# Performance work log

Hardware: AMD Instinct MI355X
Metric: run time of the kernel (lower is better)

Reference implementation:

```python
import jax, jax.numpy as jnp
import numpy as np

L, D, H, HD = 2, 2048, 16, 128          # layers, hidden, heads, head_dim
E, K, F, FS = 8, 2, 1408, 5632           # experts, top_k, moe_inter, shared_inter
V, T = 32000, 2048                       # vocab, tokens
EPS = 1e-6
ROPE_BASE = 1000000.0


def _rms(x, w):
    return x * jax.lax.rsqrt(jnp.mean(x * x, axis=-1, keepdims=True) + EPS) * w


def _rope(x, cos, sin):
    half = x.shape[-1] // 2
    x1, x2 = x[..., :half], x[..., half:]
    return jnp.concatenate([x1 * cos - x2 * sin, x1 * sin + x2 * cos], axis=-1)


def setup_inputs() -> dict:
    key = jax.random.key(0)
    ks = jax.random.split(key, 18)
    s = 0.02
    f = lambda k, shp: jax.random.normal(k, shp, jnp.float32) * s
    return {
        "input_ids": jax.random.randint(ks[0], (T,), 0, V, dtype=jnp.int32),
        "positions": jnp.arange(T, dtype=jnp.int32),
        "embed": f(ks[1], (V, D)),
        "qw": f(ks[2], (L, D, H * HD)),
        "kw": f(ks[3], (L, D, H * HD)),
        "vw": f(ks[4], (L, D, H * HD)),
        "ow": f(ks[5], (L, H * HD, D)),
        "ln1": jnp.ones((L, D), jnp.float32),
        "ln2": jnp.ones((L, D), jnp.float32),
        "router_w": f(ks[6], (L, D, E)),
        "sgate_w": f(ks[7], (L, D)),
        "wg": f(ks[8], (L, E, D, F)),
        "wu": f(ks[9], (L, E, D, F)),
        "wd": f(ks[10], (L, E, F, D)),
        "swg": f(ks[11], (L, D, FS)),
        "swu": f(ks[12], (L, D, FS)),
        "swd": f(ks[13], (L, FS, D)),
        "final_ln": jnp.ones((D,), jnp.float32),
    }


def _attn(x, positions, qw_l, kw_l, vw_l, ow_l):
    q = (x @ qw_l).reshape(T, H, HD)
    k = (x @ kw_l).reshape(T, H, HD)
    v = (x @ vw_l).reshape(T, H, HD)
    half = HD // 2
    inv = 1.0 / (ROPE_BASE ** (jnp.arange(half, dtype=jnp.float32) / half))
    ang = positions.astype(jnp.float32)[:, None] * inv[None, :]  # [T, half]
    cos, sin = jnp.cos(ang)[:, None, :], jnp.sin(ang)[:, None, :]
    q = _rope(q, cos, sin)
    k = _rope(k, cos, sin)
    scores = jnp.einsum('thd,shd->hts', q, k) * (HD ** -0.5)  # [H, T, T]
    mask = positions[:, None] >= positions[None, :]  # causal
    scores = jnp.where(mask[None], scores, -1e30)
    p = jax.nn.softmax(scores, axis=-1)
    o = jnp.einsum('hts,shd->thd', p, v).reshape(T, H * HD)
    return o @ ow_l


def _moe(x, router_w_l, sgate_w_l, wg_l, wu_l, wd_l, swg_l, swu_l, swd_l):
    # shared expert + its sigmoid gate
    sh = (jax.nn.silu(x @ swg_l) * (x @ swu_l)) @ swd_l
    sgate = jax.nn.sigmoid(x @ sgate_w_l)[:, None]
    # router: softmax in float32, then top-k with prob renorm (norm_topk_prob)
    probs = jax.nn.softmax((x @ router_w_l).astype(jnp.float32), axis=-1)
    topv, topi = jax.lax.top_k(probs, K)
    topv = topv / jnp.sum(topv, axis=-1, keepdims=True)
    combine = jnp.sum(jax.nn.one_hot(topi, E, dtype=x.dtype) * topv[..., None].astype(x.dtype), axis=1)  # [T, E]
    # dense grouped expert FFN, combined by routing weights (scatter-add equivalent)
    g = jnp.einsum('td,edf->etf', x, wg_l)
    u = jnp.einsum('td,edf->etf', x, wu_l)
    y = jnp.einsum('etf,efd->etd', jax.nn.silu(g) * u, wd_l)
    moe_out = jnp.einsum('te,etd->td', combine, y)
    return (moe_out + sgate * sh) * (1.0 / K ** 0.5)


def reference(input_ids, positions, embed, qw, kw, vw, ow, ln1, ln2, router_w,
              sgate_w, wg, wu, wd, swg, swu, swd, final_ln):
    h = embed[input_ids]  # [T, D]
    residual = None
    for l in range(L):
        if residual is None:
            residual = h
            x = _rms(h, ln1[l])
        else:
            residual = h + residual
            x = _rms(residual, ln1[l])
        h = _attn(x, positions, qw[l], kw[l], vw[l], ow[l])
        residual = h + residual
        x = _rms(residual, ln2[l])
        h = _moe(x, router_w[l], sgate_w[l], wg[l], wu[l], wd[l], swg[l], swu[l], swd[l])
    residual = h + residual
    return _rms(residual, final_ln)
```

## Files before the change

kernel.cpp:

```cpp
#include <hip/hip_runtime.h>
#include <stdint.h>

#define TT 2048
#define DD 2048
#define HH 16
#define HDIM 128
#define NE 8
#define TOPK 2
#define FF 1408
#define FSS 5632
#define NL 2

typedef __bf16 bf16;
typedef __bf16 bf16x2 __attribute__((ext_vector_type(2)));
typedef __bf16 bf16x4 __attribute__((ext_vector_type(4)));
typedef __bf16 bf16x8 __attribute__((ext_vector_type(8)));
typedef float f32x4 __attribute__((ext_vector_type(4)));

__device__ __forceinline__ void split1(float f, bf16& h, bf16& l) {
  bf16 hb = (bf16)f;
  h = hb;
  l = (bf16)(f - (float)hb);
}

__device__ __forceinline__ void gload16(const void* g, void* l) {
  __builtin_amdgcn_global_load_lds((const __attribute__((address_space(1))) void*)g,
                                   (__attribute__((address_space(3))) void*)l, 16, 0, 0);
}

template<bool LO>
__launch_bounds__(256)
__global__ void k_wtrans(const float* __restrict__ W, bf16* __restrict__ Wh,
                         bf16* __restrict__ Wl, int Kd, int N)
{
  __shared__ float T[64][68];
  const size_t slab = (size_t)blockIdx.z * (size_t)Kd * (size_t)N;
  const float* Wp = W + slab;
  const int k0 = blockIdx.x * 64, n0 = blockIdx.y * 64;
  const int tid = threadIdx.x;
  const int rr = tid >> 2, c4 = (tid & 3) * 4;
  const float* src = Wp + (size_t)(k0 + rr) * N + n0 + c4;
#pragma unroll
  for (int j = 0; j < 4; ++j) {
    f32x4 v = *(const f32x4*)(src + j * 16);
    *(f32x4*)&T[rr][c4 + j * 16] = v;
  }
  __syncthreads();
  const int nn = tid >> 2, kk = (tid & 3) * 16;
  bf16x8 h0, h1, l0, l1;
#pragma unroll
  for (int j = 0; j < 8; ++j) {
    bf16 hb, lb;
    split1(T[kk + j][nn], hb, lb);
    h0[j] = hb; l0[j] = lb;
    split1(T[kk + 8 + j][nn], hb, lb);
    h1[j] = hb; l1[j] = lb;
  }
  size_t out = slab + (size_t)(n0 + nn) * Kd + k0 + kk;
  *(bf16x8*)&Wh[out] = h0;
  *(bf16x8*)&Wh[out + 8] = h1;
  if (LO) {
    *(bf16x8*)&Wl[out] = l0;
    *(bf16x8*)&Wl[out + 8] = l1;
  }
}

template<int BMT, int NT, bool EXPERT, bool GATHER, int OM>
__launch_bounds__(256, (BMT == 128 ? 3 : 4))
__global__ void k_gemmp(const bf16* __restrict__ Ah, const bf16* __restrict__ Al,
                        const bf16* __restrict__ Bh, const bf16* __restrict__ Bl,
                        void* __restrict__ C1, void* __restrict__ C2,
                        int M, int N, int Kd, int lda, int ldc,
                        const int* __restrict__ perm, const int* __restrict__ cnt,
                        const int* __restrict__ ofs)
{
  constexpr int PL = (NT == 3) ? 2 : 1;
  constexpr int ASUB = BMT / 16;
  constexpr int AISS = PL * ASUB;
  constexpr int BISS = PL * 8;
  constexpr int QPW = (AISS + BISS) / 4;
  constexpr int IF = BMT / 32;

  int m_count = M, row_base = 0;
  size_t boff = 0;
  if (EXPERT) {
    int e = blockIdx.z;
    m_count = cnt[e];
    if ((int)(blockIdx.x * BMT) >= m_count) return;
    row_base = ofs[e];
    boff = (size_t)e * (size_t)N * (size_t)Kd;
  }
  const int tid = threadIdx.x, lane = tid & 63, wid = tid >> 6;
  const int wm = (wid >> 1) * (BMT / 2), wn = (wid & 1) * 64;
  const int lr = lane & 15, g = lane >> 4;
  const int n0 = blockIdx.y * 128;
  const int m0 = blockIdx.x * BMT;

  __shared__ bf16 As[PL][BMT][32];
  __shared__ bf16 Bs[PL][128][32];

  const bf16* srcp[QPW];
#pragma unroll
  for (int j = 0; j < QPW; ++j) {
    int q = wid * QPW + j;
    int r16 = lane >> 2;
    int kc = (lane & 3) ^ ((lane >> 3) & 3);
    if (q < AISS) {
      int pl = q / ASUB, sub = q % ASUB;
      int r = sub * 16 + r16;
      int tok;
      if (EXPERT) {
        int lrow = m0 + r;
        if (lrow >= m_count) lrow = m_count - 1;
        tok = GATHER ? perm[row_base + lrow] : (row_base + lrow);
      } else {
        tok = m0 + r;
      }
      const bf16* base = (pl == 0) ? Ah : Al;
      srcp[j] = base + (size_t)tok * lda + kc * 8;
    } else {
      int qb = q - AISS;
      int pl = qb >> 3, sub = qb & 7;
      int nrow = sub * 16 + r16;
      const bf16* base = (pl == 0) ? Bh : Bl;
      srcp[j] = base + boff + (size_t)(n0 + nrow) * Kd + kc * 8;
    }
  }

  f32x4 acc[IF][4];
#pragma unroll
  for (int i = 0; i < IF; ++i)
#pragma unroll
    for (int j = 0; j < 4; ++j)
      acc[i][j] = (f32x4){0.f, 0.f, 0.f, 0.f};

  auto ISSUE = [&](int k0) {
#pragma unroll
    for (int j = 0; j < QPW; ++j) {
      int q = wid * QPW + j;
      bf16* dst;
      if (q < AISS) {
        int pl = q / ASUB, sub = q % ASUB;
        dst = &As[pl][sub * 16][0];
      } else {
        int qb = q - AISS;
        int pl = qb >> 3, sub = qb & 7;
        dst = &Bs[pl][sub * 16][0];
      }
      gload16(srcp[j] + k0, dst);
    }
  };

  const int gs = (g ^ ((lr >> 1) & 3)) * 8;
  const int NTk = Kd >> 5;
  ISSUE(0);
  for (int t = 0; t < NTk; ++t) {
    __syncthreads();
    bf16x8 bfr[4][PL], afr[IF][PL];
#pragma unroll
    for (int jj = 0; jj < 4; ++jj)
#pragma unroll
      for (int pl = 0; pl < PL; ++pl)
        bfr[jj][pl] = *(const bf16x8*)&Bs[pl][wn + jj * 16 + lr][gs];
#pragma unroll
    for (int i = 0; i < IF; ++i)
#pragma unroll
      for (int pl = 0; pl < PL; ++pl)
        afr[i][pl] = *(const bf16x8*)&As[pl][wm + i * 16 + lr][gs];
    __syncthreads();
    if (t + 1 < NTk) ISSUE((t + 1) << 5);
#pragma unroll
    for (int i = 0; i < IF; ++i)
#pragma unroll
      for (int jj = 0; jj < 4; ++jj) {
        f32x4 a2 = acc[i][jj];
        a2 = __builtin_amdgcn_mfma_f32_16x16x32_bf16(afr[i][0], bfr[jj][0], a2, 0, 0, 0);
        if (NT == 3) {
          a2 = __builtin_amdgcn_mfma_f32_16x16x32_bf16(afr[i][0], bfr[jj][1], a2, 0, 0, 0);
          a2 = __builtin_amdgcn_mfma_f32_16x16x32_bf16(afr[i][1], bfr[jj][0], a2, 0, 0, 0);
        }
        acc[i][jj] = a2;
      }
  }

  const int r0 = g * 4;
#pragma unroll
  for (int i = 0; i < IF; ++i) {
    int lrow0 = m0 + wm + i * 16 + r0;
#pragma unroll
    for (int j = 0; j < 4; ++j) {
      int col = n0 + wn + j * 16 + lr;
      if (OM == 4) {
        bf16x4 ph, pl;
#pragma unroll
        for (int r = 0; r < 4; ++r) { bf16 hb, lb; split1(acc[i][j][r], hb, lb); ph[r] = hb; pl[r] = lb; }
        *(bf16x4*)&((bf16*)C1)[(size_t)col * ldc + lrow0] = ph;
        *(bf16x4*)&((bf16*)C2)[(size_t)col * ldc + lrow0] = pl;
      } else {
#pragma unroll
        for (int r = 0; r < 4; ++r) {
          int lrow = lrow0 + r;
          if (EXPERT && lrow >= m_count) continue;
          size_t off = (size_t)(row_base + lrow) * ldc + col;
          if (OM == 1) {
            ((float*)C1)[off] = acc[i][j][r];
          } else {
            bf16 hb, lb; split1(acc[i][j][r], hb, lb);
            ((bf16*)C1)[off] = hb;
            ((bf16*)C2)[off] = lb;
          }
        }
      }
    }
  }
}

__launch_bounds__(256)
__global__ void k_attns(const bf16* __restrict__ Qh, const bf16* __restrict__ Ql,
                        const bf16* __restrict__ Kh, const bf16* __restrict__ Kl,
                        const bf16* __restrict__ Vh, const bf16* __restrict__ Vl,
                        bf16* __restrict__ Oh, bf16* __restrict__ Ol)
{
  const int tid = threadIdx.x;
  const int lane = tid & 63, wid = tid >> 6;
  const int head = blockIdx.y;
  const int qbase = (gridDim.x - 1 - blockIdx.x) * 32;
  const int lr = lane & 15, g = lane >> 4;

  __shared__ float o_l[4][16][132];
  __shared__ float m_l[4][16], l_l[4][16];
  bf16* plbase = (bf16*)&o_l[0][0][0];
  bf16 (*pl_h)[40] = (bf16(*)[40])(plbase + wid * 16 * 40);
  bf16 (*pl_l)[40] = (bf16(*)[40])(plbase + (4 + wid) * 16 * 40);

  bf16x8 qfhA[4], qflA[4], qfhB[4], qflB[4];
  {
    size_t qoffA = (size_t)(qbase + lr) * DD + head * HDIM;
    size_t qoffB = qoffA + (size_t)16 * DD;
#pragma unroll
    for (int c = 0; c < 4; ++c) {
      qfhA[c] = *(const bf16x8*)(Qh + qoffA + c * 32 + g * 8);
      qflA[c] = *(const bf16x8*)(Ql + qoffA + c * 32 + g * 8);
      qfhB[c] = *(const bf16x8*)(Qh + qoffB + c * 32 + g * 8);
      qflB[c] = *(const bf16x8*)(Ql + qoffB + c * 32 + g * 8);
    }
  }

  f32x4 oA[8], oB[8];
#pragma unroll
  for (int d = 0; d < 8; ++d) {
    oA[d] = (f32x4){0.f, 0.f, 0.f, 0.f};
    oB[d] = (f32x4){0.f, 0.f, 0.f, 0.f};
  }
  float mA = -1e30f, lA = 0.f;
  float mB = -1e30f, lB = 0.f;

  const int qend = qbase + 32;
  for (int kb = wid * 32; kb < qend; kb += 128) {
    f32x4 sA0 = {0.f,0.f,0.f,0.f}, sA1 = {0.f,0.f,0.f,0.f};
    f32x4 sB0 = {0.f,0.f,0.f,0.f}, sB1 = {0.f,0.f,0.f,0.f};
    size_t k0off = (size_t)(kb + lr) * DD + head * HDIM;
    size_t k1off = k0off + (size_t)16 * DD;
#pragma unroll
    for (int c = 0; c < 4; ++c) {
      bf16x8 kh0 = *(const bf16x8*)(Kh + k0off + c * 32 + g * 8);
      bf16x8 kl0 = *(const bf16x8*)(Kl + k0off + c * 32 + g * 8);
      sA0 = __builtin_amdgcn_mfma_f32_16x16x32_bf16(kh0, qfhA[c], sA0, 0, 0, 0);
      sA0 = __builtin_amdgcn_mfma_f32_16x16x32_bf16(kl0, qfhA[c], sA0, 0, 0, 0);
      sA0 = __builtin_amdgcn_mfma_f32_16x16x32_bf16(kh0, qflA[c], sA0, 0, 0, 0);
      sB0 = __builtin_amdgcn_mfma_f32_16x16x32_bf16(kh0, qfhB[c], sB0, 0, 0, 0);
      sB0 = __builtin_amdgcn_mfma_f32_16x16x32_bf16(kl0, qfhB[c], sB0, 0, 0, 0);
      sB0 = __builtin_amdgcn_mfma_f32_16x16x32_bf16(kh0, qflB[c], sB0, 0, 0, 0);
      bf16x8 kh1 = *(const bf16x8*)(Kh + k1off + c * 32 + g * 8);
      bf16x8 kl1 = *(const bf16x8*)(Kl + k1off + c * 32 + g * 8);
      sA1 = __builtin_amdgcn_mfma_f32_16x16x32_bf16(kh1, qfhA[c], sA1, 0, 0, 0);
      sA1 = __builtin_amdgcn_mfma_f32_16x16x32_bf16(kl1, qfhA[c], sA1, 0, 0, 0);
      sA1 = __builtin_amdgcn_mfma_f32_16x16x32_bf16(kh1, qflA[c], sA1, 0, 0, 0);
      sB1 = __builtin_amdgcn_mfma_f32_16x16x32_bf16(kh1, qfhB[c], sB1, 0, 0, 0);
      sB1 = __builtin_amdgcn_mfma_f32_16x16x32_bf16(kl1, qfhB[c], sB1, 0, 0, 0);
      sB1 = __builtin_amdgcn_mfma_f32_16x16x32_bf16(kh1, qflB[c], sB1, 0, 0, 0);
    }
    float p0A[4], p1A[4];
    {
      float mloc = -1e30f;
      const int q = qbase + lr;
#pragma unroll
      for (int r = 0; r < 4; ++r) {
        int k0i = kb + g * 4 + r;
        float a0 = sA0[r] * 0.08838834764831845f;
        float a1 = sA1[r] * 0.08838834764831845f;
        if (k0i > q)      a0 = -1e30f;
        if (k0i + 16 > q) a1 = -1e30f;
        p0A[r] = a0; p1A[r] = a1;
        mloc = fmaxf(mloc, fmaxf(a0, a1));
      }
      mloc = fmaxf(mloc, __shfl_xor(mloc, 16, 64));
      mloc = fmaxf(mloc, __shfl_xor(mloc, 32, 64));
      float mn = fmaxf(mA, mloc);
      float alpha = __expf(mA - mn);
      mA = mn;
      float ps = 0.f;
#pragma unroll
      for (int r = 0; r < 4; ++r) {
        p0A[r] = __expf(p0A[r] - mn);
        p1A[r] = __expf(p1A[r] - mn);
        ps += p0A[r] + p1A[r];
      }
      ps += __shfl_xor(ps, 16, 64);
      ps += __shfl_xor(ps, 32, 64);
      lA = lA * alpha + ps;
      float alr[4];
#pragma unroll
      for (int r = 0; r < 4; ++r) alr[r] = __shfl(alpha, g * 4 + r, 64);
#pragma unroll
      for (int d = 0; d < 8; ++d)
#pragma unroll
        for (int r = 0; r < 4; ++r) oA[d][r] *= alr[r];
    }
    float p0B[4], p1B[4];
    {
      float mloc = -1e30f;
      const int q = qbase + 16 + lr;
#pragma unroll
      for (int r = 0; r < 4; ++r) {
        int k0i = kb + g * 4 + r;
        float a0 = sB0[r] * 0.08838834764831845f;
        float a1 = sB1[r] * 0.08838834764831845f;
        if (k0i > q)      a0 = -1e30f;
        if (k0i + 16 > q) a1 = -1e30f;
        p0B[r] = a0; p1B[r] = a1;
        mloc = fmaxf(mloc, fmaxf(a0, a1));
      }
      mloc = fmaxf(mloc, __shfl_xor(mloc, 16, 64));
      mloc = fmaxf(mloc, __shfl_xor(mloc, 32, 64));
      float mn = fmaxf(mB, mloc);
      float alpha = __expf(mB - mn);
      mB = mn;
      float ps = 0.f;
#pragma unroll
      for (int r = 0; r < 4; ++r) {
        p0B[r] = __expf(p0B[r] - mn);
        p1B[r] = __expf(p1B[r] - mn);
        ps += p0B[r] + p1B[r];
      }
      ps += __shfl_xor(ps, 16, 64);
      ps += __shfl_xor(ps, 32, 64);
      lB = lB * alpha + ps;
      float alr[4];
#pragma unroll
      for (int r = 0; r < 4; ++r) alr[r] = __shfl(alpha, g * 4 + r, 64);
#pragma unroll
      for (int d = 0; d < 8; ++d)
#pragma unroll
        for (int r = 0; r < 4; ++r) oB[d][r] *= alr[r];
    }
#pragma unroll
    for (int r = 0; r < 4; ++r) {
      bf16 hb, lb;
      split1(p0A[r], hb, lb);
      pl_h[lr][g * 4 + r] = hb;
      pl_l[lr][g * 4 + r] = lb;
      split1(p1A[r], hb, lb);
      pl_h[lr][16 + g * 4 + r] = hb;
      pl_l[lr][16 + g * 4 + r] = lb;
    }
    bf16x8 pahA = *(const bf16x8*)&pl_h[lr][g * 8];
    bf16x8 palA = *(const bf16x8*)&pl_l[lr][g * 8];
#pragma unroll
    for (int r = 0; r < 4; ++r) {
      bf16 hb, lb;
      split1(p0B[r], hb, lb);
      pl_h[lr][g * 4 + r] = hb;
      pl_l[lr][g * 4 + r] = lb;
      split1(p1B[r], hb, lb);
      pl_h[lr][16 + g * 4 + r] = hb;
      pl_l[lr][16 + g * 4 + r] = lb;
    }
    bf16x8 pahB = *(const bf16x8*)&pl_h[lr][g * 8];
    bf16x8 palB = *(const bf16x8*)&pl_l[lr][g * 8];
#pragma unroll
    for (int d = 0; d < 8; ++d) {
      size_t voff = (size_t)(head * HDIM + d * 16 + lr) * TT + kb + g * 8;
      bf16x8 vfh = *(const bf16x8*)(Vh + voff);
      bf16x8 vfl = *(const bf16x8*)(Vl + voff);
      oA[d] = __builtin_amdgcn_mfma_f32_16x16x32_bf16(pahA, vfh, oA[d], 0, 0, 0);
      oA[d] = __builtin_amdgcn_mfma_f32_16x16x32_bf16(pahA, vfl, oA[d], 0, 0, 0);
      oA[d] = __builtin_amdgcn_mfma_f32_16x16x32_bf16(palA, vfh, oA[d], 0, 0, 0);
      oB[d] = __builtin_amdgcn_mfma_f32_16x16x32_bf16(pahB, vfh, oB[d], 0, 0, 0);
      oB[d] = __builtin_amdgcn_mfma_f32_16x16x32_bf16(pahB, vfl, oB[d], 0, 0, 0);
      oB[d] = __builtin_amdgcn_mfma_f32_16x16x32_bf16(palB, vfh, oB[d], 0, 0, 0);
    }
  }

  __syncthreads();
  if (g == 0) {
    m_l[wid][lr] = mA;
    l_l[wid][lr] = lA;
  }
#pragma unroll
  for (int d = 0; d < 8; ++d)
#pragma unroll
    for (int r = 0; r < 4; ++r)
      o_l[wid][g * 4 + r][d * 16 + lr] = oA[d][r];
  __syncthreads();
  {
    const int row = tid >> 4;
    const int c0 = (tid & 15) * 8;
    float m0v = m_l[0][row], m1v = m_l[1][row], m2v = m_l[2][row], m3v = m_l[3][row];
    float ms = fmaxf(fmaxf(m0v, m1v), fmaxf(m2v, m3v));
    float s0v = __expf(m0v - ms), s1v = __expf(m1v - ms);
    float s2v = __expf(m2v - ms), s3v = __expf(m3v - ms);
    float lsum = l_l[0][row] * s0v + l_l[1][row] * s1v
               + l_l[2][row] * s2v + l_l[3][row] * s3v;
    float inv = 1.f / lsum;
    union { bf16 b[8]; uint4 u; } ph, pl;
#pragma unroll
    for (int j = 0; j < 8; ++j) {
      float v = o_l[0][row][c0 + j] * s0v + o_l[1][row][c0 + j] * s1v
              + o_l[2][row][c0 + j] * s2v + o_l[3][row][c0 + j] * s3v;
      bf16 hb, lb;
      split1(v * inv, hb, lb);
      ph.b[j] = hb; pl.b[j] = lb;
    }
    size_t oi = (size_t)(qbase + row) * DD + head * HDIM + c0;
    *(uint4*)(Oh + oi) = ph.u;
    *(uint4*)(Ol + oi) = pl.u;
  }
  __syncthreads();
  if (g == 0) {
    m_l[wid][lr] = mB;
    l_l[wid][lr] = lB;
  }
#pragma unroll
  for (int d = 0; d < 8; ++d)
#pragma unroll
    for (int r = 0; r < 4; ++r)
      o_l[wid][g * 4 + r][d * 16 + lr] = oB[d][r];
  __syncthreads();
  {
    const int row = tid >> 4;
    const int c0 = (tid & 15) * 8;
    float m0v = m_l[0][row], m1v = m_l[1][row], m2v = m_l[2][row], m3v = m_l[3][row];
    float ms = fmaxf(fmaxf(m0v, m1v), fmaxf(m2v, m3v));
    float s0v = __expf(m0v - ms), s1v = __expf(m1v - ms);
    float s2v = __expf(m2v - ms), s3v = __expf(m3v - ms);
    float lsum = l_l[0][row] * s0v + l_l[1][row] * s1v
               + l_l[2][row] * s2v + l_l[3][row] * s3v;
    float inv = 1.f / lsum;
    union { bf16 b[8]; uint4 u; } ph, pl;
#pragma unroll
    for (int j = 0; j < 8; ++j) {
      float v = o_l[0][row][c0 + j] * s0v + o_l[1][row][c0 + j] * s1v
              + o_l[2][row][c0 + j] * s2v + o_l[3][row][c0 + j] * s3v;
      bf16 hb, lb;
      split1(v * inv, hb, lb);
      ph.b[j] = hb; pl.b[j] = lb;
    }
    size_t oi = (size_t)(qbase + 16 + row) * DD + head * HDIM + c0;
    *(uint4*)(Oh + oi) = ph.u;
    *(uint4*)(Ol + oi) = pl.u;
  }
}

__global__ void k_embed(const int* __restrict__ ids, const float* __restrict__ Em,
                        float* __restrict__ Hout)
{
  int t = blockIdx.x, tid = threadIdx.x;
  const float4* s = (const float4*)(Em + (size_t)ids[t] * DD);
  float4* dst = (float4*)(Hout + (size_t)t * DD);
  dst[tid] = s[tid];
  dst[tid + 256] = s[tid + 256];
}

template<bool ADDIN, bool WF32, bool FINAL>
__launch_bounds__(256)
__global__ void k_addrms(const float* __restrict__ Hin, float* __restrict__ Res,
                         const float* __restrict__ W,
                         bf16* __restrict__ Xh, bf16* __restrict__ Xl,
                         float* __restrict__ Xf)
{
  const int t = blockIdx.x, tid = threadIdx.x;
  const size_t base = (size_t)t * DD + tid * 8;
  float x[8];
  {
    const float4* hp = (const float4*)(Hin + base);
    float4 a = hp[0], b = hp[1];
    x[0]=a.x; x[1]=a.y; x[2]=a.z; x[3]=a.w;
    x[4]=b.x; x[5]=b.y; x[6]=b.z; x[7]=b.w;
    if (ADDIN) {
      const float4* rp = (const float4*)(Res + base);
      float4 c = rp[0], d = rp[1];
      x[0]+=c.x; x[1]+=c.y; x[2]+=c.z; x[3]+=c.w;
      x[4]+=d.x; x[5]+=d.y; x[6]+=d.z; x[7]+=d.w;
    }
  }
  {
    float4* rp = (float4*)(Res + base);
    rp[0] = make_float4(x[0], x[1], x[2], x[3]);
    rp[1] = make_float4(x[4], x[5], x[6], x[7]);
  }
  float ss = 0.f;
#pragma unroll
  for (int j = 0; j < 8; ++j) ss += x[j] * x[j];
#pragma unroll
  for (int off = 32; off; off >>= 1) ss += __shfl_xor(ss, off, 64);
  __shared__ float red[4];
  if ((tid & 63) == 0) red[tid >> 6] = ss;
  __syncthreads();
  float tot = red[0] + red[1] + red[2] + red[3];
  float sc = rsqrtf(tot * (1.0f / DD) + 1e-6f);
  float y[8];
#pragma unroll
  for (int j = 0; j < 8; ++j) y[j] = x[j] * sc * W[tid * 8 + j];
  if (!FINAL) {
    union { bf16 b[8]; uint4 u; } ph, pl;
#pragma unroll
    for (int j = 0; j < 8; ++j) { bf16 hb, lb; split1(y[j], hb, lb); ph.b[j] = hb; pl.b[j] = lb; }
    *(uint4*)(Xh + base) = ph.u;
    *(uint4*)(Xl + base) = pl.u;
  }
  if (WF32 || FINAL) {
    float4* xp = (float4*)(Xf + base);
    xp[0] = make_float4(y[0], y[1], y[2], y[3]);
    xp[1] = make_float4(y[4], y[5], y[6], y[7]);
  }
}

__global__ void k_rope2(bf16* __restrict__ Qh, bf16* __restrict__ Ql,
                        bf16* __restrict__ Kh, bf16* __restrict__ Kl,
                        const int* __restrict__ pos)
{
  int idx = blockIdx.x * 256 + threadIdx.x;
  int d = idx & 63;
  int h = (idx >> 6) & (HH - 1);
  int t = idx >> 10;
  if (t >= TT) return;
  double inv = pow(1.0e6, -(double)d / 64.0);
  double ang = (double)pos[t] * inv;
  double sd, cd;
  sincos(ang, &sd, &cd);
  float sn = (float)sd, cs = (float)cd;
  size_t base = (size_t)t * DD + h * HDIM + d;
  float q1 = (float)Qh[base] + (float)Ql[base];
  float q2 = (float)Qh[base + 64] + (float)Ql[base + 64];
  float qa = q1 * cs - q2 * sn, qb = q1 * sn + q2 * cs;
  bf16 hb, lb;
  split1(qa, hb, lb); Qh[base] = hb;      Ql[base] = lb;
  split1(qb, hb, lb); Qh[base + 64] = hb; Ql[base + 64] = lb;
  float k1 = (float)Kh[base] + (float)Kl[base];
  float k2 = (float)Kh[base + 64] + (float)Kl[base + 64];
  float ka = k1 * cs - k2 * sn, kb2 = k1 * sn + k2 * cs;
  split1(ka, hb, lb);  Kh[base] = hb;      Kl[base] = lb;
  split1(kb2, hb, lb); Kh[base + 64] = hb; Kl[base + 64] = lb;
}

__launch_bounds__(64)
__global__ void k_router(const float* __restrict__ Xf, const float* __restrict__ RW,
                         const float* __restrict__ SGW, int* __restrict__ eidx,
                         float* __restrict__ ew, float* __restrict__ sgate,
                         int* __restrict__ cnt)
{
  const int t = blockIdx.x, lane = threadIdx.x;
  const float* x = Xf + (size_t)t * DD;
  float acc[8] = {0,0,0,0,0,0,0,0};
  float sg = 0.f;
  for (int i = lane; i < DD; i += 64) {
    float xv = x[i];
    const float4* w = (const float4*)(RW + (size_t)i * NE);
    float4 w0 = w[0], w1 = w[1];
    acc[0] += xv * w0.x; acc[1] += xv * w0.y; acc[2] += xv * w0.z; acc[3] += xv * w0.w;
    acc[4] += xv * w1.x; acc[5] += xv * w1.y; acc[6] += xv * w1.z; acc[7] += xv * w1.w;
    sg += xv * SGW[i];
  }
#pragma unroll
  for (int off = 32; off; off >>= 1) {
#pragma unroll
    for (int e = 0; e < 8; ++e) acc[e] += __shfl_xor(acc[e], off, 64);
    sg += __shfl_xor(sg, off, 64);
  }
  if (lane == 0) {
    int i0 = 0; float v0 = acc[0];
    for (int e = 1; e < 8; ++e) if (acc[e] > v0) { v0 = acc[e]; i0 = e; }
    int i1 = -1; float v1 = -1e30f;
    for (int e = 0; e < 8; ++e) if (e != i0 && acc[e] > v1) { v1 = acc[e]; i1 = e; }
    float w0 = 1.f / (1.f + expf(v1 - v0));
    eidx[2*t] = i0; eidx[2*t+1] = i1;
    ew[2*t] = w0; ew[2*t+1] = 1.f - w0;
    sgate[t] = 1.f / (1.f + expf(-sg));
    atomicAdd(&cnt[i0], 1);
    atomicAdd(&cnt[i1], 1);
  }
}

__global__ void k_scan(const int* __restrict__ cnt, int* __restrict__ ofs)
{
  if (threadIdx.x == 0) {
    int s = 0;
    for (int e = 0; e < NE; ++e) { ofs[e] = s; s += cnt[e]; }
    ofs[NE] = s;
  }
}

__global__ void k_assign(const int* __restrict__ eidx, const int* __restrict__ ofs,
                         int* __restrict__ cursor, int* __restrict__ perm,
                         int* __restrict__ posof)
{
  int t = blockIdx.x * 256 + threadIdx.x;
  if (t >= TT) return;
#pragma unroll
  for (int j = 0; j < 2; ++j) {
    int e = eidx[2*t + j];
    int p = ofs[e] + atomicAdd(&cursor[e], 1);
    perm[p] = t;
    posof[2*t + j] = p;
  }
}

__global__ void k_silup(const float* __restrict__ G, const float* __restrict__ U,
                        bf16* __restrict__ H, bf16* __restrict__ L)
{
  int i = (blockIdx.x * 256 + threadIdx.x) * 4;
  float4 g = *(const float4*)(G + i);
  float4 u = *(const float4*)(U + i);
  float s[4];
  s[0] = g.x / (1.f + expf(-g.x)) * u.x;
  s[1] = g.y / (1.f + expf(-g.y)) * u.y;
  s[2] = g.z / (1.f + expf(-g.z)) * u.z;
  s[3] = g.w / (1.f + expf(-g.w)) * u.w;
  bf16x4 h, l;
#pragma unroll
  for (int j = 0; j < 4; ++j) { bf16 hb, lb; split1(s[j], hb, lb); h[j] = hb; l[j] = lb; }
  *(bf16x4*)(H + i) = h;
  *(bf16x4*)(L + i) = l;
}

__global__ void k_combine(const float* __restrict__ Y, const float* __restrict__ SH,
                          const float* __restrict__ sgate, const float* __restrict__ ew,
                          const int* __restrict__ posof, float* __restrict__ Hout)
{
  int t = blockIdx.x, tid = threadIdx.x;
  int p0 = posof[2*t], p1 = posof[2*t+1];
  float w0 = ew[2*t], w1 = ew[2*t+1];
  float sgv = sgate[t];
  int d0 = tid * 8;
  const float4* a = (const float4*)(Y + (size_t)p0 * DD + d0);
  const float4* b = (const float4*)(Y + (size_t)p1 * DD + d0);
  float4 a0 = a[0], a1 = a[1], b0 = b[0], b1 = b[1];
  float y0[8] = {a0.x,a0.y,a0.z,a0.w,a1.x,a1.y,a1.z,a1.w};
  float y1[8] = {b0.x,b0.y,b0.z,b0.w,b1.x,b1.y,b1.z,b1.w};
  const float4* shp = (const float4*)(SH + (size_t)t * DD + d0);
  float4 sa = shp[0], sb = shp[1];
  float shv[8] = {sa.x, sa.y, sa.z, sa.w, sb.x, sb.y, sb.z, sb.w};
  float out[8];
#pragma unroll
  for (int j = 0; j < 8; ++j)
    out[j] = (y0[j] * w0 + y1[j] * w1 + sgv * shv[j]) * 0.70710678118654752f;
  float4* op = (float4*)(Hout + (size_t)t * DD + d0);
  op[0] = make_float4(out[0], out[1], out[2], out[3]);
  op[1] = make_float4(out[4], out[5], out[6], out[7]);
}

extern "C" void kernel_launch(void* const* d_in, const int* in_sizes, int n_in,
                              void* d_out, int out_size, void* d_ws, size_t ws_size,
                              hipStream_t stream)
{
  (void)in_sizes; (void)n_in; (void)out_size; (void)ws_size;
  const int*   ids  = (const int*)d_in[0];
  const int*   pos  = (const int*)d_in[1];
  const float* emb  = (const float*)d_in[2];
  const float* qw   = (const float*)d_in[3];
  const float* kw   = (const float*)d_in[4];
  const float* vw   = (const float*)d_in[5];
  const float* ow   = (const float*)d_in[6];
  const float* ln1  = (const float*)d_in[7];
  const float* ln2  = (const float*)d_in[8];
  const float* rw   = (const float*)d_in[9];
  const float* sgw  = (const float*)d_in[10];
  const float* wg   = (const float*)d_in[11];
  const float* wu   = (const float*)d_in[12];
  const float* wd   = (const float*)d_in[13];
  const float* swg  = (const float*)d_in[14];
  const float* swu  = (const float*)d_in[15];
  const float* swd  = (const float*)d_in[16];
  const float* fln  = (const float*)d_in[17];

  char* p = (char*)d_ws;
  auto alloc = [&](size_t b) { char* r = p; p += (b + 255) & ~(size_t)255; return r; };

  const size_t TD = (size_t)TT * DD;
  float* resid = (float*)alloc(TD * 4);
  float* hbuf  = (float*)alloc(TD * 4);
  float* xf    = (float*)alloc(TD * 4);
  bf16*  xh    = (bf16*) alloc(TD * 2);
  bf16*  xl    = (bf16*) alloc(TD * 2);
  bf16*  qhb   = (bf16*) alloc(TD * 2);
  bf16*  qlb   = (bf16*) alloc(TD * 2);
  bf16*  khb   = (bf16*) alloc(TD * 2);
  bf16*  klb   = (bf16*) alloc(TD * 2);
  bf16*  vth   = (bf16*) alloc(TD * 2);
  bf16*  vtl   = (bf16*) alloc(TD * 2);
  bf16*  aoh   = (bf16*) alloc(TD * 2);
  bf16*  aol   = (bf16*) alloc(TD * 2);
  float* shb   = (float*)alloc(TD * 4);
  const size_t SGF = (size_t)TT * FSS;
  const size_t GEF = (size_t)TT * TOPK * FF;
  bf16*  shph  = (bf16*) alloc(SGF * 2);
  bf16*  shpl  = (bf16*) alloc(SGF * 2);
  bf16*  geph  = (bf16*) alloc(GEF * 2);
  bf16*  gepl  = (bf16*) alloc(GEF * 2);
  float* region = (float*)alloc(2 * SGF * 4);
  float* sgbf = region;
  float* subf = region + SGF;
  float* gebf = region;
  float* uebf = region + GEF;
  float* ybf  = region + 2 * GEF;
  const size_t WME = (size_t)NE * DD * FF;
  bf16* wbh = (bf16*)alloc(WME * 2);
  bf16* wbl = (bf16*)alloc(WME * 2);
  int*   eidx  = (int*)  alloc((size_t)TT * TOPK * 4);
  float* ewb   = (float*)alloc((size_t)TT * TOPK * 4);
  float* sgate = (float*)alloc((size_t)TT * 4);
  int*   perm  = (int*)  alloc((size_t)TT * TOPK * 4);
  int*   posof = (int*)  alloc((size_t)TT * TOPK * 4);
  int*   cnt   = (int*)  alloc(64);
  int*   ofs   = (int*)  alloc(64);
  int*   cursor = cnt + 8;

  k_embed<<<TT, 256, 0, stream>>>(ids, emb, hbuf);

  for (int l = 0; l < NL; ++l) {
    const float* qw_l  = qw  + (size_t)l * DD * DD;
    const float* kw_l  = kw  + (size_t)l * DD * DD;
    const float* vw_l  = vw  + (size_t)l * DD * DD;
    const float* ow_l  = ow  + (size_t)l * DD * DD;
    const float* ln1_l = ln1 + (size_t)l * DD;
    const float* ln2_l = ln2 + (size_t)l * DD;
    const float* rw_l  = rw  + (size_t)l * DD * NE;
    const float* sgw_l = sgw + (size_t)l * DD;
    const float* wg_l  = wg  + (size_t)l * NE * DD * FF;
    const float* wu_l  = wu  + (size_t)l * NE * DD * FF;
    const float* wd_l  = wd  + (size_t)l * NE * FF * DD;
    const float* swg_l = swg + (size_t)l * DD * FSS;
    const float* swu_l = swu + (size_t)l * DD * FSS;
    const float* swd_l = swd + (size_t)l * FSS * DD;
    const bool last = (l == NL - 1);

    if (l == 0)
      k_addrms<false,false,false><<<TT,256,0,stream>>>(hbuf, resid, ln1_l, xh, xl, nullptr);
    else
      k_addrms<true, false,false><<<TT,256,0,stream>>>(hbuf, resid, ln1_l, xh, xl, nullptr);

    k_wtrans<true><<<dim3(32,32),256,0,stream>>>(qw_l, wbh, wbl, DD, DD);
    k_gemmp<64,3,false,false,3><<<dim3(32,16),256,0,stream>>>(xh, xl, wbh, wbl, qhb, qlb, TT, DD, DD, DD, DD, nullptr,nullptr,nullptr);
    k_wtrans<true><<<dim3(32,32),256,0,stream>>>(kw_l, wbh, wbl, DD, DD);
    k_gemmp<64,3,false,false,3><<<dim3(32,16),256,0,stream>>>(xh, xl, wbh, wbl, khb, klb, TT, DD, DD, DD, DD, nullptr,nullptr,nullptr);
    k_wtrans<true><<<dim3(32,32),256,0,stream>>>(vw_l, wbh, wbl, DD, DD);
    k_gemmp<64,3,false,false,4><<<dim3(32,16),256,0,stream>>>(xh, xl, wbh, wbl, vth, vtl, TT, DD, DD, DD, TT, nullptr,nullptr,nullptr);
    k_rope2<<<(TT*HH*64)/256, 256, 0, stream>>>(qhb, qlb, khb, klb, pos);
    k_attns<<<dim3(TT/32, HH), 256, 0, stream>>>(qhb, qlb, khb, klb, vth, vtl, aoh, aol);
    k_wtrans<true><<<dim3(32,32),256,0,stream>>>(ow_l, wbh, wbl, DD, DD);
    k_gemmp<64,3,false,false,1><<<dim3(32,16),256,0,stream>>>(aoh, aol, wbh, wbl, hbuf, nullptr, TT, DD, DD, DD, DD, nullptr,nullptr,nullptr);

    k_addrms<true,true,false><<<TT,256,0,stream>>>(hbuf, resid, ln2_l, xh, xl, xf);

    hipMemsetAsync(cnt, 0, 64, stream);
    k_router<<<TT, 64, 0, stream>>>(xf, rw_l, sgw_l, eidx, ewb, sgate, cnt);
    k_scan<<<1, 64, 0, stream>>>(cnt, ofs);
    k_assign<<<TT/256, 256, 0, stream>>>(eidx, ofs, cursor, perm, posof);

    if (!last) {
      k_wtrans<true><<<dim3(32,88),256,0,stream>>>(swg_l, wbh, wbl, DD, FSS);
      k_gemmp<128,3,false,false,1><<<dim3(16,44),256,0,stream>>>(xh, xl, wbh, wbl, sgbf, nullptr, TT, FSS, DD, DD, FSS, nullptr,nullptr,nullptr);
      k_wtrans<true><<<dim3(32,88),256,0,stream>>>(swu_l, wbh, wbl, DD, FSS);
      k_gemmp<128,3,false,false,1><<<dim3(16,44),256,0,stream>>>(xh, xl, wbh, wbl, subf, nullptr, TT, FSS, DD, DD, FSS, nullptr,nullptr,nullptr);
      k_silup<<<(TT*FSS/4)/256, 256, 0, stream>>>(sgbf, subf, shph, shpl);
      k_wtrans<true><<<dim3(88,32),256,0,stream>>>(swd_l, wbh, wbl, FSS, DD);
      k_gemmp<64,3,false,false,1><<<dim3(32,16),256,0,stream>>>(shph, shpl, wbh, wbl, shb, nullptr, TT, DD, FSS, FSS, DD, nullptr,nullptr,nullptr);
    } else {
      k_wtrans<false><<<dim3(32,88),256,0,stream>>>(swg_l, wbh, wbl, DD, FSS);
      k_gemmp<128,1,false,false,1><<<dim3(16,44),256,0,stream>>>(xh, xl, wbh, wbl, sgbf, nullptr, TT, FSS, DD, DD, FSS, nullptr,nullptr,nullptr);
      k_wtrans<false><<<dim3(32,88),256,0,stream>>>(swu_l, wbh, wbl, DD, FSS);
      k_gemmp<128,1,false,false,1><<<dim3(16,44),256,0,stream>>>(xh, xl, wbh, wbl, subf, nullptr, TT, FSS, DD, DD, FSS, nullptr,nullptr,nullptr);
      k_silup<<<(TT*FSS/4)/256, 256, 0, stream>>>(sgbf, subf, shph, shpl);
      k_wtrans<false><<<dim3(88,32),256,0,stream>>>(swd_l, wbh, wbl, FSS, DD);
      k_gemmp<64,1,false,false,1><<<dim3(32,16),256,0,stream>>>(shph, shpl, wbh, wbl, shb, nullptr, TT, DD, FSS, FSS, DD, nullptr,nullptr,nullptr);
    }

    if (!last) {
      k_wtrans<true><<<dim3(32,22,NE),256,0,stream>>>(wg_l, wbh, wbl, DD, FF);
      k_gemmp<64,3,true,true,1><<<dim3(64,11,NE),256,0,stream>>>(xh, xl, wbh, wbl, gebf, nullptr, TT, FF, DD, DD, FF, perm, cnt, ofs);
      k_wtrans<true><<<dim3(32,22,NE),256,0,stream>>>(wu_l, wbh, wbl, DD, FF);
      k_gemmp<64,3,true,true,1><<<dim3(64,11,NE),256,0,stream>>>(xh, xl, wbh, wbl, uebf, nullptr, TT, FF, DD, DD, FF, perm, cnt, ofs);
      k_silup<<<(GEF/4)/256, 256, 0, stream>>>(gebf, uebf, geph, gepl);
      k_wtrans<true><<<dim3(22,32,NE),256,0,stream>>>(wd_l, wbh, wbl, FF, DD);
      k_gemmp<64,3,true,false,1><<<dim3(64,16,NE),256,0,stream>>>(geph, gepl, wbh, wbl, ybf, nullptr, TT, DD, FF, FF, DD, nullptr, cnt, ofs);
    } else {
      k_wtrans<false><<<dim3(32,22,NE),256,0,stream>>>(wg_l, wbh, wbl, DD, FF);
      k_gemmp<64,1,true,true,1><<<dim3(64,11,NE),256,0,stream>>>(xh, xl, wbh, wbl, gebf, nullptr, TT, FF, DD, DD, FF, perm, cnt, ofs);
      k_wtrans<false><<<dim3(32,22,NE),256,0,stream>>>(wu_l, wbh, wbl, DD, FF);
      k_gemmp<64,1,true,true,1><<<dim3(64,11,NE),256,0,stream>>>(xh, xl, wbh, wbl, uebf, nullptr, TT, FF, DD, DD, FF, perm, cnt, ofs);
      k_silup<<<(GEF/4)/256, 256, 0, stream>>>(gebf, uebf, geph, gepl);
      k_wtrans<false><<<dim3(22,32,NE),256,0,stream>>>(wd_l, wbh, wbl, FF, DD);
      k_gemmp<64,1,true,false,1><<<dim3(64,16,NE),256,0,stream>>>(geph, gepl, wbh, wbl, ybf, nullptr, TT, DD, FF, FF, DD, nullptr, cnt, ofs);
    }
    k_combine<<<TT, 256, 0, stream>>>(ybf, shb, sgate, ewb, posof, hbuf);
  }

  k_addrms<true,false,true><<<TT,256,0,stream>>>(hbuf, resid, fln, nullptr, nullptr, (float*)d_out);
}
```

Baseline: 3.710 ms.

## Double GEMM K-tile to 64 with swizzled LDS and remapped block order

Raises the K step of the split-bf16 GEMM from 32 to 64, doubling the LDS tiles and using an 8-way XOR swizzle. The inner loop becomes two MFMA half-steps, and the next tile's global loads are issued after the second fragment read. This halves the number of barrier/issue iterations per K and gives more MFMA work per sync. It also permutes blockIdx.x across 8 groups to change tile scheduling order, and lowers launch bounds to 2 waves per SIMD to fit the larger LDS and register use, at the cost of occupancy.

```diff
diff --git a/kernel.cpp b/kernel.cpp
--- a/kernel.cpp
+++ b/kernel.cpp
@@ -66,7 +66,7 @@
 }
 
 template<int BMT, int NT, bool EXPERT, bool GATHER, int OM>
-__launch_bounds__(256, (BMT == 128 ? 3 : 4))
+__launch_bounds__(256, 2)
 __global__ void k_gemmp(const bf16* __restrict__ Ah, const bf16* __restrict__ Al,
                         const bf16* __restrict__ Bh, const bf16* __restrict__ Bl,
                         void* __restrict__ C1, void* __restrict__ C2,
@@ -75,18 +75,20 @@
                         const int* __restrict__ ofs)
 {
   constexpr int PL = (NT == 3) ? 2 : 1;
-  constexpr int ASUB = BMT / 16;
+  constexpr int ASUB = BMT / 8;
   constexpr int AISS = PL * ASUB;
-  constexpr int BISS = PL * 8;
+  constexpr int BISS = PL * 16;
   constexpr int QPW = (AISS + BISS) / 4;
   constexpr int IF = BMT / 32;
+
+  const int bx = ((int)blockIdx.x & 7) * ((int)gridDim.x >> 3) + ((int)blockIdx.x >> 3);
 
   int m_count = M, row_base = 0;
   size_t boff = 0;
   if (EXPERT) {
     int e = blockIdx.z;
     m_count = cnt[e];
-    if ((int)(blockIdx.x * BMT) >= m_count) return;
+    if (bx * BMT >= m_count) return;
     row_base = ofs[e];
     boff = (size_t)e * (size_t)N * (size_t)Kd;
   }
@@ -94,20 +96,20 @@
   const int wm = (wid >> 1) * (BMT / 2), wn = (wid & 1) * 64;
   const int lr = lane & 15, g = lane >> 4;
   const int n0 = blockIdx.y * 128;
-  const int m0 = blockIdx.x * BMT;
-
-  __shared__ bf16 As[PL][BMT][32];
-  __shared__ bf16 Bs[PL][128][32];
+  const int m0 = bx * BMT;
+
+  __shared__ bf16 As[PL][BMT][64];
+  __shared__ bf16 Bs[PL][128][64];
 
   const bf16* srcp[QPW];
 #pragma unroll
   for (int j = 0; j < QPW; ++j) {
     int q = wid * QPW + j;
-    int r16 = lane >> 2;
-    int kc = (lane & 3) ^ ((lane >> 3) & 3);
+    int r8 = lane >> 3;
+    int kc = (lane & 7) ^ r8;
     if (q < AISS) {
       int pl = q / ASUB, sub = q % ASUB;
-      int r = sub * 16 + r16;
+      int r = sub * 8 + r8;
       int tok;
       if (EXPERT) {
         int lrow = m0 + r;
@@ -120,8 +122,8 @@
       srcp[j] = base + (size_t)tok * lda + kc * 8;
     } else {
       int qb = q - AISS;
-      int pl = qb >> 3, sub = qb & 7;
-      int nrow = sub * 16 + r16;
+      int pl = qb >> 4, sub = qb & 15;
+      int nrow = sub * 8 + r8;
       const bf16* base = (pl == 0) ? Bh : Bl;
       srcp[j] = base + boff + (size_t)(n0 + nrow) * Kd + kc * 8;
     }
@@ -141,43 +143,67 @@
       bf16* dst;
       if (q < AISS) {
         int pl = q / ASUB, sub = q % ASUB;
-        dst = &As[pl][sub * 16][0];
+        dst = &As[pl][sub * 8][0];
       } else {
         int qb = q - AISS;
-        int pl = qb >> 3, sub = qb & 7;
-        dst = &Bs[pl][sub * 16][0];
+        int pl = qb >> 4, sub = qb & 15;
+        dst = &Bs[pl][sub * 8][0];
       }
       gload16(srcp[j] + k0, dst);
     }
   };
 
-  const int gs = (g ^ ((lr >> 1) & 3)) * 8;
-  const int NTk = Kd >> 5;
+  const int gs0 = ((0 + g) ^ (lr & 7)) * 8;
+  const int gs1 = ((4 + g) ^ (lr & 7)) * 8;
+  const int NTk = Kd >> 6;
   ISSUE(0);
   for (int t = 0; t < NTk; ++t) {
     __syncthreads();
-    bf16x8 bfr[4][PL], afr[IF][PL];
+    bf16x8 bfr0[4][PL], afr0[IF][PL];
 #pragma unroll
     for (int jj = 0; jj < 4; ++jj)
 #pragma unroll
       for (int pl = 0; pl < PL; ++pl)
-        bfr[jj][pl] = *(const bf16x8*)&Bs[pl][wn + jj * 16 + lr][gs];
+        bfr0[jj][pl] = *(const bf16x8*)&Bs[pl][wn + jj * 16 + lr][gs0];
 #pragma unroll
     for (int i = 0; i < IF; ++i)
 #pragma unroll
       for (int pl = 0; pl < PL; ++pl)
-        afr[i][pl] = *(const bf16x8*)&As[pl][wm + i * 16 + lr][gs];
-    __syncthreads();
-    if (t + 1 < NTk) ISSUE((t + 1) << 5);
+        afr0[i][pl] = *(const bf16x8*)&As[pl][wm + i * 16 + lr][gs0];
 #pragma unroll
     for (int i = 0; i < IF; ++i)
 #pragma unroll
       for (int jj = 0; jj < 4; ++jj) {
         f32x4 a2 = acc[i][jj];
-        a2 = __builtin_amdgcn_mfma_f32_16x16x32_bf16(afr[i][0], bfr[jj][0], a2, 0, 0, 0);
+        a2 = __builtin_amdgcn_mfma_f32_16x16x32_bf16(afr0[i][0], bfr0[jj][0], a2, 0, 0, 0);
         if (NT == 3) {
-          a2 = __builtin_amdgcn_mfma_f32_16x16x32_bf16(afr[i][0], bfr[jj][1], a2, 0, 0, 0);
-          a2 = __builtin_amdgcn_mfma_f32_16x16x32_bf16(afr[i][1], bfr[jj][0], a2, 0, 0, 0);
+          a2 = __builtin_amdgcn_mfma_f32_16x16x32_bf16(afr0[i][0], bfr0[jj][1], a2, 0, 0, 0);
+          a2 = __builtin_amdgcn_mfma_f32_16x16x32_bf16(afr0[i][1], bfr0[jj][0], a2, 0, 0, 0);
+        }
+        acc[i][jj] = a2;
+      }
+    bf16x8 bfr1[4][PL], afr1[IF][PL];
+#pragma unroll
+    for (int jj = 0; jj < 4; ++jj)
+#pragma unroll
+      for (int pl = 0; pl < PL; ++pl)
+        bfr1[jj][pl] = *(const bf16x8*)&Bs[pl][wn + jj * 16 + lr][gs1];
+#pragma unroll
+    for (int i = 0; i < IF; ++i)
+#pragma unroll
+      for (int pl = 0; pl < PL; ++pl)
+        afr1[i][pl] = *(const bf16x8*)&As[pl][wm + i * 16 + lr][gs1];
+    __syncthreads();
+    if (t + 1 < NTk) ISSUE((t + 1) << 6);
+#pragma unroll
+    for (int i = 0; i < IF; ++i)
+#pragma unroll
+      for (int jj = 0; jj < 4; ++jj) {
+        f32x4 a2 = acc[i][jj];
+        a2 = __builtin_amdgcn_mfma_f32_16x16x32_bf16(afr1[i][0], bfr1[jj][0], a2, 0, 0, 0);
+        if (NT == 3) {
+          a2 = __builtin_amdgcn_mfma_f32_16x16x32_bf16(afr1[i][0], bfr1[jj][1], a2, 0, 0, 0);
+          a2 = __builtin_amdgcn_mfma_f32_16x16x32_bf16(afr1[i][1], bfr1[jj][0], a2, 0, 0, 0);
         }
         acc[i][jj] = a2;
       }
```

Result: faster. 3.586 ms (-3.3%).

## Fuse QKV and shared gate/up GEMMs into single launches, swizzle M-block order

Applied to the files above, without the earlier changes.

The three attention projection weights are transposed into one concatenated buffer and computed with a single GEMM launch, with the epilogue routing each N-segment to the Q, K or transposed-V outputs. The shared-expert gate and up projections are likewise concatenated into one GEMM writing two float outputs. The GEMM also remaps blockIdx.x with an interleaving swizzle that changes which M tiles run concurrently, aimed at cache locality. The fused launches need larger weight staging buffers (3*DD and 2*FSS columns) and add epilogue branching.

```diff
diff --git a/kernel.cpp b/kernel.cpp
--- a/kernel.cpp
+++ b/kernel.cpp
@@ -31,11 +31,12 @@
 template<bool LO>
 __launch_bounds__(256)
 __global__ void k_wtrans(const float* __restrict__ W, bf16* __restrict__ Wh,
-                         bf16* __restrict__ Wl, int Kd, int N)
+                         bf16* __restrict__ Wl, int Kd, int N, int nofs, int Ntot)
 {
   __shared__ float T[64][68];
-  const size_t slab = (size_t)blockIdx.z * (size_t)Kd * (size_t)N;
-  const float* Wp = W + slab;
+  const size_t slabIn  = (size_t)blockIdx.z * (size_t)Kd * (size_t)N;
+  const size_t slabOut = (size_t)blockIdx.z * (size_t)Kd * (size_t)Ntot;
+  const float* Wp = W + slabIn;
   const int k0 = blockIdx.x * 64, n0 = blockIdx.y * 64;
   const int tid = threadIdx.x;
   const int rr = tid >> 2, c4 = (tid & 3) * 4;
@@ -56,7 +57,7 @@
     split1(T[kk + 8 + j][nn], hb, lb);
     h1[j] = hb; l1[j] = lb;
   }
-  size_t out = slab + (size_t)(n0 + nn) * Kd + k0 + kk;
+  size_t out = slabOut + (size_t)(nofs + n0 + nn) * Kd + k0 + kk;
   *(bf16x8*)&Wh[out] = h0;
   *(bf16x8*)&Wh[out + 8] = h1;
   if (LO) {
@@ -70,6 +71,8 @@
 __global__ void k_gemmp(const bf16* __restrict__ Ah, const bf16* __restrict__ Al,
                         const bf16* __restrict__ Bh, const bf16* __restrict__ Bl,
                         void* __restrict__ C1, void* __restrict__ C2,
+                        void* __restrict__ C3, void* __restrict__ C4,
+                        void* __restrict__ C5, void* __restrict__ C6,
                         int M, int N, int Kd, int lda, int ldc,
                         const int* __restrict__ perm, const int* __restrict__ cnt,
                         const int* __restrict__ ofs)
@@ -81,12 +84,14 @@
   constexpr int QPW = (AISS + BISS) / 4;
   constexpr int IF = BMT / 32;
 
+  const int bx = ((int)blockIdx.x & 7) * ((int)gridDim.x >> 3) + ((int)blockIdx.x >> 3);
+
   int m_count = M, row_base = 0;
   size_t boff = 0;
   if (EXPERT) {
     int e = blockIdx.z;
     m_count = cnt[e];
-    if ((int)(blockIdx.x * BMT) >= m_count) return;
+    if (bx * BMT >= m_count) return;
     row_base = ofs[e];
     boff = (size_t)e * (size_t)N * (size_t)Kd;
   }
@@ -94,7 +99,7 @@
   const int wm = (wid >> 1) * (BMT / 2), wn = (wid & 1) * 64;
   const int lr = lane & 15, g = lane >> 4;
   const int n0 = blockIdx.y * 128;
-  const int m0 = blockIdx.x * BMT;
+  const int m0 = bx * BMT;
 
   __shared__ bf16 As[PL][BMT][32];
   __shared__ bf16 Bs[PL][128][32];
@@ -183,31 +188,45 @@
       }
   }
 
+  void *O1 = C1, *O2 = C2;
+  bool otrans = (OM == 4);
+  int coff = 0;
+  if (OM == 5) {
+    int seg = n0 / ldc;
+    coff = seg * ldc;
+    if (seg == 1)      { O1 = C3; O2 = C4; }
+    else if (seg == 2) { O1 = C5; O2 = C6; otrans = true; }
+  } else if (OM == 6) {
+    int seg = n0 / ldc;
+    coff = seg * ldc;
+    if (seg) O1 = C3;
+  }
+
   const int r0 = g * 4;
 #pragma unroll
   for (int i = 0; i < IF; ++i) {
     int lrow0 = m0 + wm + i * 16 + r0;
 #pragma unroll
     for (int j = 0; j < 4; ++j) {
-      int col = n0 + wn + j * 16 + lr;
-      if (OM == 4) {
+      int col = n0 + wn + j * 16 + lr - coff;
+      if (OM == 4 || (OM == 5 && otrans)) {
         bf16x4 ph, pl;
 #pragma unroll
         for (int r = 0; r < 4; ++r) { bf16 hb, lb; split1(acc[i][j][r], hb, lb); ph[r] = hb; pl[r] = lb; }
-        *(bf16x4*)&((bf16*)C1)[(size_t)col * ldc + lrow0] = ph;
-        *(bf16x4*)&((bf16*)C2)[(size_t)col * ldc + lrow0] = pl;
+        *(bf16x4*)&((bf16*)O1)[(size_t)col * ldc + lrow0] = ph;
+        *(bf16x4*)&((bf16*)O2)[(size_t)col * ldc + lrow0] = pl;
       } else {
 #pragma unroll
         for (int r = 0; r < 4; ++r) {
           int lrow = lrow0 + r;
           if (EXPERT && lrow >= m_count) continue;
           size_t off = (size_t)(row_base + lrow) * ldc + col;
-          if (OM == 1) {
-            ((float*)C1)[off] = acc[i][j][r];
+          if (OM == 1 || OM == 6) {
+            ((float*)O1)[off] = acc[i][j][r];
           } else {
             bf16 hb, lb; split1(acc[i][j][r], hb, lb);
-            ((bf16*)C1)[off] = hb;
-            ((bf16*)C2)[off] = lb;
+            ((bf16*)O1)[off] = hb;
+            ((bf16*)O2)[off] = lb;
           }
         }
       }
@@ -750,16 +769,16 @@
     else
       k_addrms<true, false,false><<<TT,256,0,stream>>>(hbuf, resid, ln1_l, xh, xl, nullptr);
 
-    k_wtrans<true><<<dim3(32,32),256,0,stream>>>(qw_l, wbh, wbl, DD, DD);
-    k_gemmp<64,3,false,false,3><<<dim3(32,16),256,0,stream>>>(xh, xl, wbh, wbl, qhb, qlb, TT, DD, DD, DD, DD, nullptr,nullptr,nullptr);
-    k_wtrans<true><<<dim3(32,32),256,0,stream>>>(kw_l, wbh, wbl, DD, DD);
-    k_gemmp<64,3,false,false,3><<<dim3(32,16),256,0,stream>>>(xh, xl, wbh, wbl, khb, klb, TT, DD, DD, DD, DD, nullptr,nullptr,nullptr);
-    k_wtrans<true><<<dim3(32,32),256,0,stream>>>(vw_l, wbh, wbl, DD, DD);
-    k_gemmp<64,3,false,false,4><<<dim3(32,16),256,0,stream>>>(xh, xl, wbh, wbl, vth, vtl, TT, DD, DD, DD, TT, nullptr,nullptr,nullptr);
+    k_wtrans<true><<<dim3(32,32),256,0,stream>>>(qw_l, wbh, wbl, DD, DD, 0,    3*DD);
+    k_wtrans<true><<<dim3(32,32),256,0,stream>>>(kw_l, wbh, wbl, DD, DD, DD,   3*DD);
+    k_wtrans<true><<<dim3(32,32),256,0,stream>>>(vw_l, wbh, wbl, DD, DD, 2*DD, 3*DD);
+    k_gemmp<64,3,false,false,5><<<dim3(32,48),256,0,stream>>>(xh, xl, wbh, wbl,
+        qhb, qlb, khb, klb, vth, vtl, TT, 3*DD, DD, DD, DD, nullptr,nullptr,nullptr);
     k_rope2<<<(TT*HH*64)/256, 256, 0, stream>>>(qhb, qlb, khb, klb, pos);
     k_attns<<<dim3(TT/32, HH), 256, 0, stream>>>(qhb, qlb, khb, klb, vth, vtl, aoh, aol);
-    k_wtrans<true><<<dim3(32,32),256,0,stream>>>(ow_l, wbh, wbl, DD, DD);
-    k_gemmp<64,3,false,false,1><<<dim3(32,16),256,0,stream>>>(aoh, aol, wbh, wbl, hbuf, nullptr, TT, DD, DD, DD, DD, nullptr,nullptr,nullptr);
+    k_wtrans<true><<<dim3(32,32),256,0,stream>>>(ow_l, wbh, wbl, DD, DD, 0, DD);
+    k_gemmp<64,3,false,false,1><<<dim3(32,16),256,0,stream>>>(aoh, aol, wbh, wbl,
+        hbuf, nullptr, nullptr, nullptr, nullptr, nullptr, TT, DD, DD, DD, DD, nullptr,nullptr,nullptr);
 
     k_addrms<true,true,false><<<TT,256,0,stream>>>(hbuf, resid, ln2_l, xh, xl, xf);
 
@@ -769,39 +788,47 @@
     k_assign<<<TT/256, 256, 0, stream>>>(eidx, ofs, cursor, perm, posof);
 
     if (!last) {
-      k_wtrans<true><<<dim3(32,88),256,0,stream>>>(swg_l, wbh, wbl, DD, FSS);
-      k_gemmp<128,3,false,false,1><<<dim3(16,44),256,0,stream>>>(xh, xl, wbh, wbl, sgbf, nullptr, TT, FSS, DD, DD, FSS, nullptr,nullptr,nullptr);
-      k_wtrans<true><<<dim3(32,88),256,0,stream>>>(swu_l, wbh, wbl, DD, FSS);
-      k_gemmp<128,3,false,false,1><<<dim3(16,44),256,0,stream>>>(xh, xl, wbh, wbl, subf, nullptr, TT, FSS, DD, DD, FSS, nullptr,nullptr,nullptr);
+      k_wtrans<true><<<dim3(32,88),256,0,stream>>>(swg_l, wbh, wbl, DD, FSS, 0,   2*FSS);
+      k_wtrans<true><<<dim3(32,88),256,0,stream>>>(swu_l, wbh, wbl, DD, FSS, FSS, 2*FSS);
+      k_gemmp<128,3,false,false,6><<<dim3(16,88),256,0,stream>>>(xh, xl, wbh, wbl,
+          sgbf, nullptr, subf, nullptr, nullptr, nullptr, TT, 2*FSS, DD, DD, FSS, nullptr,nullptr,nullptr);
       k_silup<<<(TT*FSS/4)/256, 256, 0, stream>>>(sgbf, subf, shph, shpl);
-      k_wtrans<true><<<dim3(88,32),256,0,stream>>>(swd_l, wbh, wbl, FSS, DD);
-      k_gemmp<64,3,false,false,1><<<dim3(32,16),256,0,stream>>>(shph, shpl, wbh, wbl, shb, nullptr, TT, DD, FSS, FSS, DD, nullptr,nullptr,nullptr);
+      k_wtrans<true><<<dim3(88,32),256,0,stream>>>(swd_l, wbh, wbl, FSS, DD, 0, DD);
+      k_gemmp<64,3,false,false,1><<<dim3(32,16),256,0,stream>>>(shph, shpl, wbh, wbl,
+          shb, nullptr, nullptr, nullptr, nullptr, nullptr, TT, DD, FSS, FSS, DD, nullptr,nullptr,nullptr);
     } else {
-      k_wtrans<false><<<dim3(32,88),256,0,stream>>>(swg_l, wbh, wbl, DD, FSS);
-      k_gemmp<128,1,false,false,1><<<dim3(16,44),256,0,stream>>>(xh, xl, wbh, wbl, sgbf, nullptr, TT, FSS, DD, DD, FSS, nullptr,nullptr,nullptr);
-      k_wtrans<false><<<dim3(32,88),256,0,stream>>>(swu_l, wbh, wbl, DD, FSS);
-      k_gemmp<128,1,false,false,1><<<dim3(16,44),256,0,stream>>>(xh, xl, wbh, wbl, subf, nullptr, TT, FSS, DD, DD, FSS, nullptr,nullptr,nullptr);
+      k_wtrans<false><<<dim3(32,88),256,0,stream>>>(swg_l, wbh, wbl, DD, FSS, 0,   2*FSS);
+      k_wtrans<false><<<dim3(32,88),256,0,stream>>>(swu_l, wbh, wbl, DD, FSS, FSS, 2*FSS);
+      k_gemmp<128,1,false,false,6><<<dim3(16,88),256,0,stream>>>(xh, xl, wbh, wbl,
+          sgbf, nullptr, subf, nullptr, nullptr, nullptr, TT, 2*FSS, DD, DD, FSS, nullptr,nullptr,nullptr);
       k_silup<<<(TT*FSS/4)/256, 256, 0, stream>>>(sgbf, subf, shph, shpl);
-      k_wtrans<false><<<dim3(88,32),256,0,stream>>>(swd_l, wbh, wbl, FSS, DD);
-      k_gemmp<64,1,false,false,1><<<dim3(32,16),256,0,stream>>>(shph, shpl, wbh, wbl, shb, nullptr, TT, DD, FSS, FSS, DD, nullptr,nullptr,nullptr);
+      k_wtrans<false><<<dim3(88,32),256,0,stream>>>(swd_l, wbh, wbl, FSS, DD, 0, DD);
+      k_gemmp<64,1,false,false,1><<<dim3(32,16),256,0,stream>>>(shph, shpl, wbh, wbl,
+          shb, nullptr, nullptr, nullptr, nullptr, nullptr, TT, DD, FSS, FSS, DD, nullptr,nullptr,nullptr);
     }
 
     if (!last) {
-      k_wtrans<true><<<dim3(32,22,NE),256,0,stream>>>(wg_l, wbh, wbl, DD, FF);
-      k_gemmp<64,3,true,true,1><<<dim3(64,11,NE),256,0,stream>>>(xh, xl, wbh, wbl, gebf, nullptr, TT, FF, DD, DD, FF, perm, cnt, ofs);
-      k_wtrans<true><<<dim3(32,22,NE),256,0,stream>>>(wu_l, wbh, wbl, DD, FF);
-      k_gemmp<64,3,true,true,1><<<dim3(64,11,NE),256,0,stream>>>(xh, xl, wbh, wbl, uebf, nullptr, TT, FF, DD, DD, FF, perm, cnt, ofs);
+      k_wtrans<true><<<dim3(32,22,NE),256,0,stream>>>(wg_l, wbh, wbl, DD, FF, 0, FF);
+      k_gemmp<64,3,true,true,1><<<dim3(64,11,NE),256,0,stream>>>(xh, xl, wbh, wbl,
+          gebf, nullptr, nullptr, nullptr, nullptr, nullptr, TT, FF, DD, DD, FF, perm, cnt, ofs);
+      k_wtrans<true><<<dim3(32,22,NE),256,0,stream>>>(wu_l, wbh, wbl, DD, FF, 0, FF);
+      k_gemmp<64,3,true,true,1><<<dim3(64,11,NE),256,0,stream>>>(xh, xl, wbh, wbl,
+          uebf, nullptr, nullptr, nullptr, nullptr, nullptr, TT, FF, DD, DD, FF, perm, cnt, ofs);
       k_silup<<<(GEF/4)/256, 256, 0, stream>>>(gebf, uebf, geph, gepl);
-      k_wtrans<true><<<dim3(22,32,NE),256,0,stream>>>(wd_l, wbh, wbl, FF, DD);
-      k_gemmp<64,3,true,false,1><<<dim3(64,16,NE),256,0,stream>>>(geph, gepl, wbh, wbl, ybf, nullptr, TT, DD, FF, FF, DD, nullptr, cnt, ofs);
+      k_wtrans<true><<<dim3(22,32,NE),256,0,stream>>>(wd_l, wbh, wbl, FF, DD, 0, DD);
+      k_gemmp<64,3,true,false,1><<<dim3(64,16,NE),256,0,stream>>>(geph, gepl, wbh, wbl,
+          ybf, nullptr, nullptr, nullptr, nullptr, nullptr, TT, DD, FF, FF, DD, nullptr, cnt, ofs);
     } else {
-      k_wtrans<false><<<dim3(32,22,NE),256,0,stream>>>(wg_l, wbh, wbl, DD, FF);
-      k_gemmp<64,1,true,true,1><<<dim3(64,11,NE),256,0,stream>>>(xh, xl, wbh, wbl, gebf, nullptr, TT, FF, DD, DD, FF, perm, cnt, ofs);
-      k_wtrans<false><<<dim3(32,22,NE),256,0,stream>>>(wu_l, wbh, wbl, DD, FF);
-      k_gemmp<64,1,true,true,1><<<dim3(64,11,NE),256,0,stream>>>(xh, xl, wbh, wbl, uebf, nullptr, TT, FF, DD, DD, FF, perm, cnt, ofs);
+      k_wtrans<false><<<dim3(32,22,NE),256,0,stream>>>(wg_l, wbh, wbl, DD, FF, 0, FF);
+      k_gemmp<64,1,true,true,1><<<dim3(64,11,NE),256,0,stream>>>(xh, xl, wbh, wbl,
+          gebf, nullptr, nullptr, nullptr, nullptr, nullptr, TT, FF, DD, DD, FF, perm, cnt, ofs);
+      k_wtrans<false><<<dim3(32,22,NE),256,0,stream>>>(wu_l, wbh, wbl, DD, FF, 0, FF);
+      k_gemmp<64,1,true,true,1><<<dim3(64,11,NE),256,0,stream>>>(xh, xl, wbh, wbl,
+          uebf, nullptr, nullptr, nullptr, nullptr, nullptr, TT, FF, DD, DD, FF, perm, cnt, ofs);
       k_silup<<<(GEF/4)/256, 256, 0, stream>>>(gebf, uebf, geph, gepl);
-      k_wtrans<false><<<dim3(22,32,NE),256,0,stream>>>(wd_l, wbh, wbl, FF, DD);
-      k_gemmp<64,1,true,false,1><<<dim3(64,16,NE),256,0,stream>>>(geph, gepl, wbh, wbl, ybf, nullptr, TT, DD, FF, FF, DD, nullptr, cnt, ofs);
+      k_wtrans<false><<<dim3(22,32,NE),256,0,stream>>>(wd_l, wbh, wbl, FF, DD, 0, DD);
+      k_gemmp<64,1,true,false,1><<<dim3(64,16,NE),256,0,stream>>>(geph, gepl, wbh, wbl,
+          ybf, nullptr, nullptr, nullptr, nullptr, nullptr, TT, DD, FF, FF, DD, nullptr, cnt, ofs);
     }
     k_combine<<<TT, 256, 0, stream>>>(ybf, shb, sgate, ewb, posof, hbuf);
   }
```

Result: slower. 4.616 ms (+24.4%).
